# Kernel tuning notes

Measured on AMD Instinct MI355X. Metric: run time of the kernel, lower is better.

## Reference

```python
import jax, jax.numpy as jnp
import numpy as np

LN_EPS = 1e-5

def _layernorm(x, g, b):
    m = jnp.mean(x, axis=-1, keepdims=True)
    v = jnp.var(x, axis=-1, keepdims=True)
    return (x - m) * jax.lax.rsqrt(v + LN_EPS) * g + b

def setup_inputs() -> dict:
    key = jax.random.key(0)
    ks = jax.random.split(key, 12)
    BT, D, OH, OW = 32, 768, 28, 43
    N, NFB, NFC = 12, 1024, 256
    s = 0.02
    return {
        "roi_feature": jax.random.normal(ks[0], (BT * N, NFB), jnp.float32),
        "image_feature": jax.random.normal(ks[1], (BT, D, OH, OW), jnp.float32),
        "conv_w": jax.random.normal(ks[2], (NFC, D), jnp.float32) * s,
        "conv_b": jnp.zeros((NFC,), jnp.float32),
        "emb_w": jax.random.normal(ks[3], (NFC, NFB), jnp.float32) * s,
        "emb_b": jnp.zeros((NFC,), jnp.float32),
        "ln1_g": jnp.ones((NFC,), jnp.float32),
        "ln1_b": jnp.zeros((NFC,), jnp.float32),
        "ffn_w1": jax.random.normal(ks[4], (NFC, NFC), jnp.float32) * s,
        "ffn_b1": jnp.zeros((NFC,), jnp.float32),
        "ffn_w2": jax.random.normal(ks[5], (NFC, NFC), jnp.float32) * s,
        "ffn_b2": jnp.zeros((NFC,), jnp.float32),
        "ln2_g": jnp.ones((NFC,), jnp.float32),
        "ln2_b": jnp.zeros((NFC,), jnp.float32),
        "N": 12,
        "layer_id": 1,
    }

def reference(roi_feature, image_feature, conv_w, conv_b, emb_w, emb_b,
              ln1_g, ln1_b, ffn_w1, ffn_b1, ffn_w2, ffn_b2, ln2_g, ln2_b,
              N, layer_id):
    BT, D, OH, OW = image_feature.shape
    NFC = conv_w.shape[0]
    # 1x1 conv == channel GEMM: [BT, D, OH, OW] -> [BT, NFC, OH*OW]
    img = jnp.einsum('bchw,oc->bohw', image_feature, conv_w) + conv_b[None, :, None, None]
    img = img.reshape(BT, NFC, OH * OW)                       # [BT, NFC, P]
    # roi embedding: [BT*N, NFB] -> [BT, N, NFC]
    emb = (roi_feature @ emb_w.T + emb_b).reshape(BT, N, NFC)
    # cross-attention: logits [BT, N, P], softmax over spatial positions
    logits = jnp.einsum('bnc,bcp->bnp', emb, img)
    A = jax.nn.softmax(logits, axis=2)
    ctx = jnp.einsum('bnp,bcp->bnc', A, img).reshape(BT * N, NFC)
    # residual + LN1 (dropout is identity at inference)
    x = _layernorm(ctx + emb.reshape(BT * N, NFC), ln1_g, ln1_b)
    # FFN residual + LN2
    h = jax.nn.relu(x @ ffn_w1.T + ffn_b1) @ ffn_w2.T + ffn_b2
    return _layernorm(x + h, ln2_g, ln2_b)
```

## Files before the change

### kernel.cpp

```cpp
#include <hip/hip_runtime.h>
#include <hip/hip_bf16.h>
#include <stdint.h>

typedef __hip_bfloat16 bf16;
typedef __attribute__((ext_vector_type(8))) __bf16 frag8;
typedef __attribute__((ext_vector_type(4))) float f32x4;

#define GLDS16(gsrc, ldst)                                                        \
  __builtin_amdgcn_global_load_lds(                                               \
      (const __attribute__((address_space(1))) void*)(gsrc),                      \
      (__attribute__((address_space(3))) void*)(ldst), 16, 0, 0)

__device__ inline float wred_sum(float v) {
#pragma unroll
  for (int o = 32; o; o >>= 1) v += __shfl_down(v, o);
  return v;
}
__device__ inline float wred_max(float v) {
#pragma unroll
  for (int o = 32; o; o >>= 1) v = fmaxf(v, __shfl_down(v, o));
  return v;
}
__device__ inline unsigned short bits_of(bf16 h) { return *(unsigned short*)&h; }
__device__ inline unsigned pack2(float x, float y) {
  return (unsigned)bits_of(__float2bfloat16(x)) |
         ((unsigned)bits_of(__float2bfloat16(y)) << 16);
}
__device__ inline frag8 cvt8(float4 lo, float4 hi) {
  union { frag8 f; unsigned short u[8]; } r;
  r.u[0] = bits_of(__float2bfloat16(lo.x));
  r.u[1] = bits_of(__float2bfloat16(lo.y));
  r.u[2] = bits_of(__float2bfloat16(lo.z));
  r.u[3] = bits_of(__float2bfloat16(lo.w));
  r.u[4] = bits_of(__float2bfloat16(hi.x));
  r.u[5] = bits_of(__float2bfloat16(hi.y));
  r.u[6] = bits_of(__float2bfloat16(hi.z));
  r.u[7] = bits_of(__float2bfloat16(hi.w));
  return r.f;
}

__global__ __launch_bounds__(256) void convert_cw(const float* __restrict__ s,
                                                  bf16* __restrict__ d, int n) {
  int i = blockIdx.x * 256 + threadIdx.x;
  if (i < n) d[i] = __float2bfloat16(s[i]);
}

__global__ __launch_bounds__(256) void transpose_x(const float* __restrict__ X,
                                                   bf16* __restrict__ Xt) {
  __shared__ float t[64][65];
  int b = blockIdx.z;
  int p0 = blockIdx.x * 64, c0 = blockIdx.y * 64;
  int tid = threadIdx.x;
  int cr = tid >> 4, p4 = (tid & 15) * 4;
#pragma unroll
  for (int r = 0; r < 4; ++r) {
    int c = cr + r * 16;
    float4 v = make_float4(0.f, 0.f, 0.f, 0.f);
    if (p0 + p4 < 1204)
      v = *(const float4*)(X + ((long)b * 768 + c0 + c) * 1204 + p0 + p4);
    t[c][p4] = v.x; t[c][p4 + 1] = v.y; t[c][p4 + 2] = v.z; t[c][p4 + 3] = v.w;
  }
  __syncthreads();
  int cl = (tid & 31) * 2, pr = tid >> 5;
#pragma unroll
  for (int r = 0; r < 8; ++r) {
    int pl = pr + r * 8;
    unsigned u = pack2(t[cl][pl], t[cl + 1][pl]);
    *(unsigned*)(Xt + ((long)b * 1280 + p0 + pl) * 768 + c0 + cl) = u;
  }
}

__global__ __launch_bounds__(256) void conv_gemm(
    const bf16* __restrict__ W, const bf16* __restrict__ Xt,
    bf16* __restrict__ img, const float* __restrict__ bias) {
  int bid = blockIdx.x;
  int xcd = bid & 7, slot = bid >> 3;
  int mrun = slot & 1;
  int q = (slot >> 1) + xcd * 40;
  int nx = q % 10, bz = q / 10;
  int n0 = nx * 128, m0 = mrun * 128;
  const int K = 768;
  const bf16* Ab = W + (long)m0 * K;
  const bf16* Bb = Xt + (long)bz * 1280 * K + (long)n0 * K;
  __shared__ __align__(16) bf16 lA[128 * 32];
  __shared__ __align__(16) bf16 lB[128 * 32];
  int tid = threadIdx.x;
  int w = tid >> 6, lane = tid & 63;
  int wm = w >> 1, wn = w & 1;
  int lr = lane & 15, kg = lane >> 4;
  f32x4 acc[4][4] = {};
  for (int k0 = 0; k0 < K; k0 += 32) {
#pragma unroll
    for (int i = 0; i < 2; ++i) {
      int off = w * 2048 + i * 1024 + lane * 16;
      int row = off >> 6, kb = off & 63;
      long gbyte = (long)row * (K * 2) + (long)k0 * 2 + kb;
      GLDS16((const char*)Ab + gbyte, (char*)lA + w * 2048 + i * 1024);
      GLDS16((const char*)Bb + gbyte, (char*)lB + w * 2048 + i * 1024);
    }
    __syncthreads();
    frag8 af[4], bv[4];
#pragma unroll
    for (int mi = 0; mi < 4; ++mi)
      af[mi] = *(const frag8*)((const char*)lA + (wm * 64 + mi * 16 + lr) * 64 + kg * 16);
#pragma unroll
    for (int ni = 0; ni < 4; ++ni)
      bv[ni] = *(const frag8*)((const char*)lB + (wn * 64 + ni * 16 + lr) * 64 + kg * 16);
#pragma unroll
    for (int mi = 0; mi < 4; ++mi)
#pragma unroll
      for (int ni = 0; ni < 4; ++ni)
        acc[mi][ni] = __builtin_amdgcn_mfma_f32_16x16x32_bf16(af[mi], bv[ni], acc[mi][ni], 0, 0, 0);
    __syncthreads();
  }
#pragma unroll
  for (int mi = 0; mi < 4; ++mi)
#pragma unroll
    for (int ni = 0; ni < 4; ++ni)
#pragma unroll
      for (int j = 0; j < 4; ++j) {
        int o = m0 + wm * 64 + mi * 16 + kg * 4 + j;
        int p = n0 + wn * 64 + ni * 16 + lr;
        float v = acc[mi][ni][j] + bias[o];
        img[((long)bz * 256 + o) * 1280 + p] = __float2bfloat16(v);
      }
}

template <bool AF32, bool BF32, bool RELU, bool OUT_BF16>
__global__ __launch_bounds__(64) void gemm_sm2(const void* __restrict__ Av,
                                               const void* __restrict__ Bv,
                                               void* __restrict__ C, int K,
                                               const float* __restrict__ bias) {
  int n0 = blockIdx.x * 64, m0 = blockIdx.y * 64;
  int lr = threadIdx.x & 15, kg = threadIdx.x >> 4;
  f32x4 acc[4][4] = {};
#pragma unroll 2
  for (int k0 = 0; k0 < K; k0 += 32) {
    frag8 af[4], bv[4];
#pragma unroll
    for (int mi = 0; mi < 4; ++mi) {
      long row = m0 + mi * 16 + lr;
      if constexpr (AF32) {
        const float* ap = (const float*)Av + row * K + k0 + kg * 8;
        af[mi] = cvt8(*(const float4*)ap, *(const float4*)(ap + 4));
      } else {
        af[mi] = *(const frag8*)((const bf16*)Av + row * K + k0 + kg * 8);
      }
    }
#pragma unroll
    for (int ni = 0; ni < 4; ++ni) {
      long row = n0 + ni * 16 + lr;
      if constexpr (BF32) {
        const float* bp = (const float*)Bv + row * K + k0 + kg * 8;
        bv[ni] = cvt8(*(const float4*)bp, *(const float4*)(bp + 4));
      } else {
        bv[ni] = *(const frag8*)((const bf16*)Bv + row * K + k0 + kg * 8);
      }
    }
#pragma unroll
    for (int mi = 0; mi < 4; ++mi)
#pragma unroll
      for (int ni = 0; ni < 4; ++ni)
        acc[mi][ni] = __builtin_amdgcn_mfma_f32_16x16x32_bf16(af[mi], bv[ni],
                                                              acc[mi][ni], 0, 0, 0);
  }
#pragma unroll
  for (int mi = 0; mi < 4; ++mi)
#pragma unroll
    for (int ni = 0; ni < 4; ++ni)
#pragma unroll
      for (int j = 0; j < 4; ++j) {
        int row = m0 + mi * 16 + kg * 4 + j;
        int col = n0 + ni * 16 + lr;
        float v = acc[mi][ni][j] + bias[col];
        if (RELU) v = fmaxf(v, 0.f);
        long idx = (long)row * 256 + col;
        if constexpr (OUT_BF16) ((bf16*)C)[idx] = __float2bfloat16(v);
        else ((float*)C)[idx] = v;
      }
}

__global__ __launch_bounds__(256) void logits_k(const bf16* __restrict__ img,
                                                const float* __restrict__ emb,
                                                float* __restrict__ lgt) {
  int b = blockIdx.x;
  __shared__ float e[3072];
  const float* eb = emb + (long)b * 3072;
  for (int i = threadIdx.x; i < 3072; i += 256) e[i] = eb[i];
  __syncthreads();
  int p = blockIdx.y * 256 + threadIdx.x;
  if (p >= 1204) return;
  const bf16* ib = img + (long)b * 256 * 1280 + p;
  float acc[12] = {};
#pragma unroll 4
  for (int c = 0; c < 256; ++c) {
    float xv = __bfloat162float(ib[(long)c * 1280]);
#pragma unroll
    for (int n = 0; n < 12; ++n) acc[n] += e[n * 256 + c] * xv;
  }
#pragma unroll
  for (int n = 0; n < 12; ++n) lgt[((long)b * 12 + n) * 1204 + p] = acc[n];
}

__global__ __launch_bounds__(256) void softmax_k(const float* __restrict__ lgt,
                                                 bf16* __restrict__ am) {
  int b = blockIdx.x, n = blockIdx.y, tid = threadIdx.x;
  bf16* row = am + ((long)b * 16 + n) * 1280;
  if (n >= 12) {
    for (int i = tid; i < 1280; i += 256) row[i] = __float2bfloat16(0.f);
    return;
  }
  const float* lr = lgt + ((long)b * 12 + n) * 1204;
  float vals[5];
  float m = -3.0e38f;
#pragma unroll
  for (int i = 0; i < 5; ++i) {
    int pp = tid + i * 256;
    vals[i] = (pp < 1204) ? lr[pp] : -3.0e38f;
    m = fmaxf(m, vals[i]);
  }
  m = wred_max(m);
  __shared__ float rd[4];
  int w = tid >> 6, lane = tid & 63;
  if (lane == 0) rd[w] = m;
  __syncthreads();
  m = fmaxf(fmaxf(rd[0], rd[1]), fmaxf(rd[2], rd[3]));
  float s = 0.f;
#pragma unroll
  for (int i = 0; i < 5; ++i) {
    int pp = tid + i * 256;
    vals[i] = (pp < 1204) ? __expf(vals[i] - m) : 0.f;
    s += vals[i];
  }
  s = wred_sum(s);
  __syncthreads();
  if (lane == 0) rd[w] = s;
  __syncthreads();
  s = rd[0] + rd[1] + rd[2] + rd[3];
  float inv = 1.f / s;
#pragma unroll
  for (int i = 0; i < 5; ++i) {
    int pp = tid + i * 256;
    row[pp] = __float2bfloat16((pp < 1204) ? vals[i] * inv : 0.f);
  }
}

__global__ __launch_bounds__(256) void ctx_split(const bf16* __restrict__ img,
                                                 const bf16* __restrict__ am,
                                                 float* __restrict__ cpart) {
  int b = blockIdx.x, kc = blockIdx.y;
  const bf16* Ab = img + (long)b * 256 * 1280;
  const bf16* Bb = am + (long)b * 16 * 1280;
  __shared__ __align__(16) bf16 lA[256 * 32];
  __shared__ __align__(16) bf16 lB[16 * 32];
  int tid = threadIdx.x, w = tid >> 6, lane = tid & 63;
  int lr = lane & 15, kg = lane >> 4;
  f32x4 acc[4] = {};
  int kend = kc * 128 + 128;
  for (int k0 = kc * 128; k0 < kend; k0 += 32) {
#pragma unroll
    for (int i = 0; i < 4; ++i) {
      int off = w * 4096 + i * 1024 + lane * 16;
      int row = off >> 6, kb = off & 63;
      GLDS16((const char*)Ab + (long)row * 2560 + k0 * 2 + kb,
             (char*)lA + w * 4096 + i * 1024);
    }
    if (w == 0) {
      int off = lane * 16, row = off >> 6, kb = off & 63;
      GLDS16((const char*)Bb + (long)row * 2560 + k0 * 2 + kb, (char*)lB);
    }
    __syncthreads();
    frag8 bv = *(const frag8*)((const char*)lB + lr * 64 + kg * 16);
#pragma unroll
    for (int mi = 0; mi < 4; ++mi) {
      frag8 av = *(const frag8*)((const char*)lA + (w * 64 + mi * 16 + lr) * 64 + kg * 16);
      acc[mi] = __builtin_amdgcn_mfma_f32_16x16x32_bf16(av, bv, acc[mi], 0, 0, 0);
    }
    __syncthreads();
  }
  int n = lr;
  if (n < 12) {
#pragma unroll
    for (int mi = 0; mi < 4; ++mi)
#pragma unroll
      for (int j = 0; j < 4; ++j)
        cpart[((long)kc * 384 + b * 12 + n) * 256 + (w * 64 + mi * 16 + kg * 4 + j)] =
            acc[mi][j];
  }
}

__global__ __launch_bounds__(256) void ln_k(const float* __restrict__ a, int nparts,
                                            long pstride, const float* __restrict__ bb,
                                            const float* __restrict__ g,
                                            const float* __restrict__ be,
                                            float* __restrict__ of) {
  int r = blockIdx.x, c = threadIdx.x;
  long idx = (long)r * 256 + c;
  float v = bb[idx];
  for (int q = 0; q < nparts; ++q) v += a[idx + q * pstride];
  float s = wred_sum(v);
  float s2 = wred_sum(v * v);
  __shared__ float r1[4], r2[4];
  int w = c >> 6, lane = c & 63;
  if (lane == 0) { r1[w] = s; r2[w] = s2; }
  __syncthreads();
  float st = r1[0] + r1[1] + r1[2] + r1[3];
  float s2t = r2[0] + r2[1] + r2[2] + r2[3];
  float mean = st * (1.f / 256.f);
  float var = s2t * (1.f / 256.f) - mean * mean;
  float rs = rsqrtf(var + 1e-5f);
  of[idx] = (v - mean) * rs * g[c] + be[c];
}

extern "C" void kernel_launch(void* const* d_in, const int* in_sizes, int n_in,
                              void* d_out, int out_size, void* d_ws, size_t ws_size,
                              hipStream_t stream) {
  const float* roi   = (const float*)d_in[0];
  const float* imgf  = (const float*)d_in[1];
  const float* convw = (const float*)d_in[2];
  const float* convb = (const float*)d_in[3];
  const float* embw  = (const float*)d_in[4];
  const float* embb  = (const float*)d_in[5];
  const float* ln1g  = (const float*)d_in[6];
  const float* ln1b  = (const float*)d_in[7];
  const float* w1    = (const float*)d_in[8];
  const float* b1    = (const float*)d_in[9];
  const float* w2    = (const float*)d_in[10];
  const float* b2    = (const float*)d_in[11];
  const float* ln2g  = (const float*)d_in[12];
  const float* ln2b  = (const float*)d_in[13];
  float* out = (float*)d_out;

  char* p = (char*)d_ws;
  size_t off = 0;
  auto take = [&](size_t sz) -> char* {
    char* r = p + off;
    off += (sz + 255) & ~(size_t)255;
    return r;
  };
  bf16*  img   = (bf16*)take((size_t)32 * 256 * 1280 * 2);
  bf16*  Xt    = (bf16*)take((size_t)32 * 1280 * 768 * 2);
  bf16*  cwb   = (bf16*)take((size_t)256 * 768 * 2);
  float* emb   = (float*)take((size_t)384 * 256 * 4);
  float* lgt   = (float*)take((size_t)384 * 1204 * 4);
  bf16*  am    = (bf16*)take((size_t)32 * 16 * 1280 * 2);
  float* cpart = (float*)take((size_t)10 * 384 * 256 * 4);
  float* x     = (float*)take((size_t)384 * 256 * 4);
  bf16*  h1    = (bf16*)take((size_t)384 * 256 * 2);
  float* h     = (float*)take((size_t)384 * 256 * 4);

  gemm_sm2<true, true, false, false><<<dim3(4, 6), 64, 0, stream>>>(
      roi, embw, emb, 1024, embb);
  convert_cw<<<(196608 + 255) / 256, 256, 0, stream>>>(convw, cwb, 196608);
  transpose_x<<<dim3(20, 12, 32), 256, 0, stream>>>(imgf, Xt);
  conv_gemm<<<640, 256, 0, stream>>>(cwb, Xt, img, convb);
  logits_k<<<dim3(32, 5), 256, 0, stream>>>(img, emb, lgt);
  softmax_k<<<dim3(32, 16), 256, 0, stream>>>(lgt, am);
  ctx_split<<<dim3(32, 10), 256, 0, stream>>>(img, am, cpart);
  ln_k<<<384, 256, 0, stream>>>(cpart, 10, (long)384 * 256, emb, ln1g, ln1b, x);
  gemm_sm2<true, true, true, true><<<dim3(4, 6), 64, 0, stream>>>(
      x, w1, h1, 256, b1);
  gemm_sm2<false, true, false, false><<<dim3(4, 6), 64, 0, stream>>>(
      h1, w2, h, 256, b2);
  ln_k<<<384, 256, 0, stream>>>(h, 1, 0, x, ln2g, ln2b, out);
}
```

Measured before the change: 166.8 us.

## Reassociate 1x1 conv into attention to avoid materializing conv output

The full conv GEMM over image features is replaced by folding the conv weight into the query side (emb·W gives an effective 768-dim query) and into the output side (attention-weighted raw features are multiplied by W afterwards). Logits and context are computed directly from the fp32 image features, so the transpose, the bf16 conversion and the large conv GEMM go away. The conv bias is dropped from the logits, which is valid because it only shifts each softmax row by a constant. In exchange, the image features are streamed twice in fp32 and small split-K partial buffers are added.

After: 258.5 us. 1.55x slower.

```diff
diff --git a/kernel.cpp b/kernel.cpp
--- a/kernel.cpp
+++ b/kernel.cpp
@@ -6,11 +6,6 @@
 typedef __attribute__((ext_vector_type(8))) __bf16 frag8;
 typedef __attribute__((ext_vector_type(4))) float f32x4;
 
-#define GLDS16(gsrc, ldst)                                                        \
-  __builtin_amdgcn_global_load_lds(                                               \
-      (const __attribute__((address_space(1))) void*)(gsrc),                      \
-      (__attribute__((address_space(3))) void*)(ldst), 16, 0, 0)
-
 __device__ inline float wred_sum(float v) {
 #pragma unroll
   for (int o = 32; o; o >>= 1) v += __shfl_down(v, o);
@@ -22,10 +17,6 @@
   return v;
 }
 __device__ inline unsigned short bits_of(bf16 h) { return *(unsigned short*)&h; }
-__device__ inline unsigned pack2(float x, float y) {
-  return (unsigned)bits_of(__float2bfloat16(x)) |
-         ((unsigned)bits_of(__float2bfloat16(y)) << 16);
-}
 __device__ inline frag8 cvt8(float4 lo, float4 hi) {
   union { frag8 f; unsigned short u[8]; } r;
   r.u[0] = bits_of(__float2bfloat16(lo.x));
@@ -39,97 +30,24 @@
   return r.f;
 }
 
-__global__ __launch_bounds__(256) void convert_cw(const float* __restrict__ s,
-                                                  bf16* __restrict__ d, int n) {
-  int i = blockIdx.x * 256 + threadIdx.x;
-  if (i < n) d[i] = __float2bfloat16(s[i]);
-}
-
-__global__ __launch_bounds__(256) void transpose_x(const float* __restrict__ X,
-                                                   bf16* __restrict__ Xt) {
-  __shared__ float t[64][65];
-  int b = blockIdx.z;
-  int p0 = blockIdx.x * 64, c0 = blockIdx.y * 64;
-  int tid = threadIdx.x;
-  int cr = tid >> 4, p4 = (tid & 15) * 4;
-#pragma unroll
-  for (int r = 0; r < 4; ++r) {
-    int c = cr + r * 16;
-    float4 v = make_float4(0.f, 0.f, 0.f, 0.f);
-    if (p0 + p4 < 1204)
-      v = *(const float4*)(X + ((long)b * 768 + c0 + c) * 1204 + p0 + p4);
-    t[c][p4] = v.x; t[c][p4 + 1] = v.y; t[c][p4 + 2] = v.z; t[c][p4 + 3] = v.w;
-  }
-  __syncthreads();
-  int cl = (tid & 31) * 2, pr = tid >> 5;
-#pragma unroll
-  for (int r = 0; r < 8; ++r) {
-    int pl = pr + r * 8;
-    unsigned u = pack2(t[cl][pl], t[cl + 1][pl]);
-    *(unsigned*)(Xt + ((long)b * 1280 + p0 + pl) * 768 + c0 + cl) = u;
-  }
-}
-
-__global__ __launch_bounds__(256) void conv_gemm(
-    const bf16* __restrict__ W, const bf16* __restrict__ Xt,
-    bf16* __restrict__ img, const float* __restrict__ bias) {
-  int bid = blockIdx.x;
-  int xcd = bid & 7, slot = bid >> 3;
-  int mrun = slot & 1;
-  int q = (slot >> 1) + xcd * 40;
-  int nx = q % 10, bz = q / 10;
-  int n0 = nx * 128, m0 = mrun * 128;
-  const int K = 768;
-  const bf16* Ab = W + (long)m0 * K;
-  const bf16* Bb = Xt + (long)bz * 1280 * K + (long)n0 * K;
-  __shared__ __align__(16) bf16 lA[128 * 32];
-  __shared__ __align__(16) bf16 lB[128 * 32];
-  int tid = threadIdx.x;
-  int w = tid >> 6, lane = tid & 63;
-  int wm = w >> 1, wn = w & 1;
-  int lr = lane & 15, kg = lane >> 4;
-  f32x4 acc[4][4] = {};
-  for (int k0 = 0; k0 < K; k0 += 32) {
-#pragma unroll
-    for (int i = 0; i < 2; ++i) {
-      int off = w * 2048 + i * 1024 + lane * 16;
-      int row = off >> 6, kb = off & 63;
-      long gbyte = (long)row * (K * 2) + (long)k0 * 2 + kb;
-      GLDS16((const char*)Ab + gbyte, (char*)lA + w * 2048 + i * 1024);
-      GLDS16((const char*)Bb + gbyte, (char*)lB + w * 2048 + i * 1024);
-    }
-    __syncthreads();
-    frag8 af[4], bv[4];
-#pragma unroll
-    for (int mi = 0; mi < 4; ++mi)
-      af[mi] = *(const frag8*)((const char*)lA + (wm * 64 + mi * 16 + lr) * 64 + kg * 16);
-#pragma unroll
-    for (int ni = 0; ni < 4; ++ni)
-      bv[ni] = *(const frag8*)((const char*)lB + (wn * 64 + ni * 16 + lr) * 64 + kg * 16);
-#pragma unroll
-    for (int mi = 0; mi < 4; ++mi)
-#pragma unroll
-      for (int ni = 0; ni < 4; ++ni)
-        acc[mi][ni] = __builtin_amdgcn_mfma_f32_16x16x32_bf16(af[mi], bv[ni], acc[mi][ni], 0, 0, 0);
-    __syncthreads();
-  }
-#pragma unroll
-  for (int mi = 0; mi < 4; ++mi)
-#pragma unroll
-    for (int ni = 0; ni < 4; ++ni)
-#pragma unroll
-      for (int j = 0; j < 4; ++j) {
-        int o = m0 + wm * 64 + mi * 16 + kg * 4 + j;
-        int p = n0 + wn * 64 + ni * 16 + lr;
-        float v = acc[mi][ni][j] + bias[o];
-        img[((long)bz * 256 + o) * 1280 + p] = __float2bfloat16(v);
-      }
-}
-
-template <bool AF32, bool BF32, bool RELU, bool OUT_BF16>
+__global__ __launch_bounds__(256) void wt_k(const float* __restrict__ W,
+                                            bf16* __restrict__ Wt) {
+  __shared__ float t[32][33];
+  int c0 = blockIdx.x * 32, o0 = blockIdx.y * 32;
+  int tx = threadIdx.x & 31, ty = threadIdx.x >> 5;
+#pragma unroll
+  for (int i = 0; i < 4; ++i)
+    t[ty + i * 8][tx] = W[(long)(o0 + ty + i * 8) * 768 + c0 + tx];
+  __syncthreads();
+#pragma unroll
+  for (int i = 0; i < 4; ++i)
+    Wt[(long)(c0 + ty + i * 8) * 256 + o0 + tx] = __float2bfloat16(t[tx][ty + i * 8]);
+}
+
+template <bool AF32, bool BF32, bool RELU, bool OUT_BF16, bool BIAS>
 __global__ __launch_bounds__(64) void gemm_sm2(const void* __restrict__ Av,
                                                const void* __restrict__ Bv,
-                                               void* __restrict__ C, int K,
+                                               void* __restrict__ C, int K, int ldc,
                                                const float* __restrict__ bias) {
   int n0 = blockIdx.x * 64, m0 = blockIdx.y * 64;
   int lr = threadIdx.x & 15, kg = threadIdx.x >> 4;
@@ -172,51 +90,54 @@
       for (int j = 0; j < 4; ++j) {
         int row = m0 + mi * 16 + kg * 4 + j;
         int col = n0 + ni * 16 + lr;
-        float v = acc[mi][ni][j] + bias[col];
+        float v = acc[mi][ni][j];
+        if (BIAS) v += bias[col];
         if (RELU) v = fmaxf(v, 0.f);
-        long idx = (long)row * 256 + col;
+        long idx = (long)row * ldc + col;
         if constexpr (OUT_BF16) ((bf16*)C)[idx] = __float2bfloat16(v);
         else ((float*)C)[idx] = v;
       }
 }
 
-__global__ __launch_bounds__(256) void logits_k(const bf16* __restrict__ img,
-                                                const float* __restrict__ emb,
-                                                float* __restrict__ lgt) {
-  int b = blockIdx.x;
-  __shared__ float e[3072];
-  const float* eb = emb + (long)b * 3072;
-  for (int i = threadIdx.x; i < 3072; i += 256) e[i] = eb[i];
-  __syncthreads();
-  int p = blockIdx.y * 256 + threadIdx.x;
+__global__ __launch_bounds__(256) void logits2(const float* __restrict__ X,
+                                               const float* __restrict__ embW,
+                                               float* __restrict__ lgt) {
+  int px = blockIdx.x, cs = blockIdx.y, b = blockIdx.z;
+  __shared__ float e[12 * 384];
+  for (int i = threadIdx.x; i < 12 * 384; i += 256)
+    e[i] = embW[((long)b * 12 + i / 384) * 768 + cs * 384 + (i % 384)];
+  __syncthreads();
+  int p = px * 256 + threadIdx.x;
   if (p >= 1204) return;
-  const bf16* ib = img + (long)b * 256 * 1280 + p;
+  const float* xb = X + ((long)b * 768 + cs * 384) * 1204 + p;
   float acc[12] = {};
-#pragma unroll 4
-  for (int c = 0; c < 256; ++c) {
-    float xv = __bfloat162float(ib[(long)c * 1280]);
-#pragma unroll
-    for (int n = 0; n < 12; ++n) acc[n] += e[n * 256 + c] * xv;
-  }
-#pragma unroll
-  for (int n = 0; n < 12; ++n) lgt[((long)b * 12 + n) * 1204 + p] = acc[n];
-}
-
-__global__ __launch_bounds__(256) void softmax_k(const float* __restrict__ lgt,
-                                                 bf16* __restrict__ am) {
+#pragma unroll 8
+  for (int c = 0; c < 384; ++c) {
+    float xv = xb[(long)c * 1204];
+#pragma unroll
+    for (int n = 0; n < 12; ++n) acc[n] += e[n * 384 + c] * xv;
+  }
+#pragma unroll
+  for (int n = 0; n < 12; ++n)
+    lgt[((long)cs * 384 + b * 12 + n) * 1204 + p] = acc[n];
+}
+
+__global__ __launch_bounds__(256) void softmax2(const float* __restrict__ lgt,
+                                                bf16* __restrict__ am) {
   int b = blockIdx.x, n = blockIdx.y, tid = threadIdx.x;
   bf16* row = am + ((long)b * 16 + n) * 1280;
   if (n >= 12) {
     for (int i = tid; i < 1280; i += 256) row[i] = __float2bfloat16(0.f);
     return;
   }
-  const float* lr = lgt + ((long)b * 12 + n) * 1204;
+  const float* l0 = lgt + ((long)b * 12 + n) * 1204;
+  const float* l1 = l0 + (long)384 * 1204;
   float vals[5];
   float m = -3.0e38f;
 #pragma unroll
   for (int i = 0; i < 5; ++i) {
     int pp = tid + i * 256;
-    vals[i] = (pp < 1204) ? lr[pp] : -3.0e38f;
+    vals[i] = (pp < 1204) ? (l0[pp] + l1[pp]) : -3.0e38f;
     m = fmaxf(m, vals[i]);
   }
   m = wred_max(m);
@@ -245,59 +166,97 @@
   }
 }
 
-__global__ __launch_bounds__(256) void ctx_split(const bf16* __restrict__ img,
-                                                 const bf16* __restrict__ am,
-                                                 float* __restrict__ cpart) {
-  int b = blockIdx.x, kc = blockIdx.y;
-  const bf16* Ab = img + (long)b * 256 * 1280;
-  const bf16* Bb = am + (long)b * 16 * 1280;
-  __shared__ __align__(16) bf16 lA[256 * 32];
-  __shared__ __align__(16) bf16 lB[16 * 32];
-  int tid = threadIdx.x, w = tid >> 6, lane = tid & 63;
-  int lr = lane & 15, kg = lane >> 4;
+__global__ __launch_bounds__(64) void ctx_a(const float* __restrict__ X,
+                                            const bf16* __restrict__ am,
+                                            float* __restrict__ Yp) {
+  int ct = blockIdx.x, kc = blockIdx.y, b = blockIdx.z;
+  int c0 = ct * 64;
+  int kst = kc * 256, kend = min(kst + 256, 1204);
+  int lr = threadIdx.x & 15, kg = threadIdx.x >> 4;
   f32x4 acc[4] = {};
-  int kend = kc * 128 + 128;
-  for (int k0 = kc * 128; k0 < kend; k0 += 32) {
-#pragma unroll
-    for (int i = 0; i < 4; ++i) {
-      int off = w * 4096 + i * 1024 + lane * 16;
-      int row = off >> 6, kb = off & 63;
-      GLDS16((const char*)Ab + (long)row * 2560 + k0 * 2 + kb,
-             (char*)lA + w * 4096 + i * 1024);
-    }
-    if (w == 0) {
-      int off = lane * 16, row = off >> 6, kb = off & 63;
-      GLDS16((const char*)Bb + (long)row * 2560 + k0 * 2 + kb, (char*)lB);
-    }
-    __syncthreads();
-    frag8 bv = *(const frag8*)((const char*)lB + lr * 64 + kg * 16);
+  for (int k0 = kst; k0 < kend; k0 += 32) {
+    frag8 bv = *(const frag8*)(am + ((long)b * 16 + lr) * 1280 + k0 + kg * 8);
+    bool full = (k0 + 32 <= 1204);
 #pragma unroll
     for (int mi = 0; mi < 4; ++mi) {
-      frag8 av = *(const frag8*)((const char*)lA + (w * 64 + mi * 16 + lr) * 64 + kg * 16);
+      const float* ap = X + ((long)b * 768 + c0 + mi * 16 + lr) * 1204 + k0 + kg * 8;
+      frag8 av;
+      if (full) {
+        av = cvt8(*(const float4*)ap, *(const float4*)(ap + 4));
+      } else {
+        float t[8];
+#pragma unroll
+        for (int j = 0; j < 8; ++j)
+          t[j] = (k0 + kg * 8 + j < 1204) ? ap[j] : 0.f;
+        av = cvt8(make_float4(t[0], t[1], t[2], t[3]),
+                  make_float4(t[4], t[5], t[6], t[7]));
+      }
       acc[mi] = __builtin_amdgcn_mfma_f32_16x16x32_bf16(av, bv, acc[mi], 0, 0, 0);
     }
-    __syncthreads();
-  }
-  int n = lr;
-  if (n < 12) {
+  }
+  if (lr < 12) {
+#pragma unroll
+    for (int mi = 0; mi < 4; ++mi) {
+      long base = (((long)kc * 32 + b) * 12 + lr) * 768 + c0 + mi * 16 + kg * 4;
+      *(float4*)&Yp[base] = make_float4(acc[mi][0], acc[mi][1], acc[mi][2], acc[mi][3]);
+    }
+  }
+}
+
+__global__ __launch_bounds__(64) void ctx_gemm(const float* __restrict__ Yp,
+                                               const float* __restrict__ W,
+                                               float* __restrict__ C,
+                                               const float* __restrict__ bias) {
+  const long QS = (long)32 * 12 * 768;
+  int n0 = blockIdx.x * 64, m0 = blockIdx.y * 64;
+  int lr = threadIdx.x & 15, kg = threadIdx.x >> 4;
+  f32x4 acc[4][4] = {};
+  for (int k0 = 0; k0 < 768; k0 += 32) {
+    frag8 af[4], bv[4];
+#pragma unroll
+    for (int mi = 0; mi < 4; ++mi) {
+      const float* ap = Yp + (long)(m0 + mi * 16 + lr) * 768 + k0 + kg * 8;
+      float4 lo = *(const float4*)ap, hi = *(const float4*)(ap + 4);
+#pragma unroll
+      for (int q = 1; q < 5; ++q) {
+        float4 l2 = *(const float4*)(ap + q * QS), h2 = *(const float4*)(ap + q * QS + 4);
+        lo.x += l2.x; lo.y += l2.y; lo.z += l2.z; lo.w += l2.w;
+        hi.x += h2.x; hi.y += h2.y; hi.z += h2.z; hi.w += h2.w;
+      }
+      af[mi] = cvt8(lo, hi);
+    }
+#pragma unroll
+    for (int ni = 0; ni < 4; ++ni) {
+      const float* bp = W + (long)(n0 + ni * 16 + lr) * 768 + k0 + kg * 8;
+      bv[ni] = cvt8(*(const float4*)bp, *(const float4*)(bp + 4));
+    }
 #pragma unroll
     for (int mi = 0; mi < 4; ++mi)
 #pragma unroll
-      for (int j = 0; j < 4; ++j)
-        cpart[((long)kc * 384 + b * 12 + n) * 256 + (w * 64 + mi * 16 + kg * 4 + j)] =
-            acc[mi][j];
-  }
-}
-
-__global__ __launch_bounds__(256) void ln_k(const float* __restrict__ a, int nparts,
-                                            long pstride, const float* __restrict__ bb,
+      for (int ni = 0; ni < 4; ++ni)
+        acc[mi][ni] = __builtin_amdgcn_mfma_f32_16x16x32_bf16(af[mi], bv[ni],
+                                                              acc[mi][ni], 0, 0, 0);
+  }
+#pragma unroll
+  for (int mi = 0; mi < 4; ++mi)
+#pragma unroll
+    for (int ni = 0; ni < 4; ++ni)
+#pragma unroll
+      for (int j = 0; j < 4; ++j) {
+        int row = m0 + mi * 16 + kg * 4 + j;
+        int col = n0 + ni * 16 + lr;
+        C[(long)row * 256 + col] = acc[mi][ni][j] + bias[col];
+      }
+}
+
+__global__ __launch_bounds__(256) void ln_k(const float* __restrict__ a,
+                                            const float* __restrict__ bb,
                                             const float* __restrict__ g,
                                             const float* __restrict__ be,
                                             float* __restrict__ of) {
   int r = blockIdx.x, c = threadIdx.x;
   long idx = (long)r * 256 + c;
-  float v = bb[idx];
-  for (int q = 0; q < nparts; ++q) v += a[idx + q * pstride];
+  float v = a[idx] + bb[idx];
   float s = wred_sum(v);
   float s2 = wred_sum(v * v);
   __shared__ float r1[4], r2[4];
@@ -338,29 +297,30 @@
     off += (sz + 255) & ~(size_t)255;
     return r;
   };
-  bf16*  img   = (bf16*)take((size_t)32 * 256 * 1280 * 2);
-  bf16*  Xt    = (bf16*)take((size_t)32 * 1280 * 768 * 2);
-  bf16*  cwb   = (bf16*)take((size_t)256 * 768 * 2);
-  float* emb   = (float*)take((size_t)384 * 256 * 4);
-  float* lgt   = (float*)take((size_t)384 * 1204 * 4);
-  bf16*  am    = (bf16*)take((size_t)32 * 16 * 1280 * 2);
-  float* cpart = (float*)take((size_t)10 * 384 * 256 * 4);
-  float* x     = (float*)take((size_t)384 * 256 * 4);
-  bf16*  h1    = (bf16*)take((size_t)384 * 256 * 2);
-  float* h     = (float*)take((size_t)384 * 256 * 4);
-
-  gemm_sm2<true, true, false, false><<<dim3(4, 6), 64, 0, stream>>>(
-      roi, embw, emb, 1024, embb);
-  convert_cw<<<(196608 + 255) / 256, 256, 0, stream>>>(convw, cwb, 196608);
-  transpose_x<<<dim3(20, 12, 32), 256, 0, stream>>>(imgf, Xt);
-  conv_gemm<<<640, 256, 0, stream>>>(cwb, Xt, img, convb);
-  logits_k<<<dim3(32, 5), 256, 0, stream>>>(img, emb, lgt);
-  softmax_k<<<dim3(32, 16), 256, 0, stream>>>(lgt, am);
-  ctx_split<<<dim3(32, 10), 256, 0, stream>>>(img, am, cpart);
-  ln_k<<<384, 256, 0, stream>>>(cpart, 10, (long)384 * 256, emb, ln1g, ln1b, x);
-  gemm_sm2<true, true, true, true><<<dim3(4, 6), 64, 0, stream>>>(
-      x, w1, h1, 256, b1);
-  gemm_sm2<false, true, false, false><<<dim3(4, 6), 64, 0, stream>>>(
-      h1, w2, h, 256, b2);
-  ln_k<<<384, 256, 0, stream>>>(h, 1, 0, x, ln2g, ln2b, out);
-}
+  float* emb  = (float*)take((size_t)384 * 256 * 4);
+  bf16*  Wt   = (bf16*)take((size_t)768 * 256 * 2);
+  float* embW = (float*)take((size_t)384 * 768 * 4);
+  float* lgt  = (float*)take((size_t)2 * 384 * 1204 * 4);
+  bf16*  am   = (bf16*)take((size_t)32 * 16 * 1280 * 2);
+  float* Yp   = (float*)take((size_t)5 * 32 * 12 * 768 * 4);
+  float* ctxf = (float*)take((size_t)384 * 256 * 4);
+  float* x    = (float*)take((size_t)384 * 256 * 4);
+  bf16*  h1   = (bf16*)take((size_t)384 * 256 * 2);
+  float* h    = (float*)take((size_t)384 * 256 * 4);
+
+  gemm_sm2<true, true, false, false, true><<<dim3(4, 6), 64, 0, stream>>>(
+      roi, embw, emb, 1024, 256, embb);
+  wt_k<<<dim3(24, 8), 256, 0, stream>>>(convw, Wt);
+  gemm_sm2<true, false, false, false, false><<<dim3(12, 6), 64, 0, stream>>>(
+      emb, Wt, embW, 256, 768, nullptr);
+  logits2<<<dim3(5, 2, 32), 256, 0, stream>>>(imgf, embW, lgt);
+  softmax2<<<dim3(32, 16), 256, 0, stream>>>(lgt, am);
+  ctx_a<<<dim3(12, 5, 32), 64, 0, stream>>>(imgf, am, Yp);
+  ctx_gemm<<<dim3(4, 6), 64, 0, stream>>>(Yp, convw, ctxf, convb);
+  ln_k<<<384, 256, 0, stream>>>(ctxf, emb, ln1g, ln1b, x);
+  gemm_sm2<true, true, true, true, true><<<dim3(4, 6), 64, 0, stream>>>(
+      x, w1, h1, 256, 256, b1);
+  gemm_sm2<false, true, false, false, true><<<dim3(4, 6), 64, 0, stream>>>(
+      h1, w2, h, 256, 256, b2);
+  ln_k<<<384, 256, 0, stream>>>(h, x, ln2g, ln2b, out);
+}
```
